# Performance work log

Measured on AMD Instinct MI355X. Metric: run time of the kernel, lower is better.

Reference implementation:

```python
import jax, jax.numpy as jnp
import numpy as np


def conv2d(x, w, b, pad=0, groups=1):
    y = jax.lax.conv_general_dilated(
        x, w, (1, 1), [(pad, pad), (pad, pad)],
        dimension_numbers=('NCHW', 'OIHW', 'NCHW'), feature_group_count=groups)
    return y + b[None, :, None, None]


def layernorm(x, w, b, eps=1e-5):
    # per-pixel LayerNorm over channel dim (matches to_3d -> nn.LayerNorm(dim) -> to_4d)
    mu = x.mean(1, keepdims=True)
    var = ((x - mu) ** 2).mean(1, keepdims=True)
    return (x - mu) * jax.lax.rsqrt(var + eps) * w[None, :, None, None] + b[None, :, None, None]


def setup_inputs():
    key = jax.random.key(0)
    ks = jax.random.split(key, 16)
    B, C, H, W = 1, 64, 64, 64
    heads, dh = 8, 8
    inner = heads * dh          # 64
    hid_lc = 32                 # max(16, inner // 2)
    hid_f = 4 * C               # 256, ffn_expansion_factor = 4
    def s(k, shape, fan):
        return (jax.random.normal(k, shape, jnp.float32) / np.float32(np.sqrt(fan)))
    return {
        'x': jax.random.normal(ks[0], (B, C, H, W), jnp.float32),
        'luma': jax.random.uniform(ks[1], (B, 1, H, W), jnp.float32),
        'ln1_w': jnp.ones((C,), jnp.float32), 'ln1_b': jnp.zeros((C,), jnp.float32),
        'qkv_w': s(ks[2], (3 * inner, C, 1, 1), C), 'qkv_b': jnp.zeros((3 * inner,), jnp.float32),
        'proj_w': s(ks[3], (C, inner, 1, 1), inner), 'proj_b': jnp.zeros((C,), jnp.float32),
        'lc1_w': s(ks[4], (hid_lc, 1, 3, 3), 9), 'lc1_b': jnp.zeros((hid_lc,), jnp.float32),
        'lc2_w': s(ks[5], (hid_lc, hid_lc, 3, 3), 9 * hid_lc), 'lc2_b': jnp.zeros((hid_lc,), jnp.float32),
        'gam_w': s(ks[6], (inner, hid_lc, 1, 1), hid_lc), 'gam_b': jnp.zeros((inner,), jnp.float32),
        'bet_w': s(ks[7], (inner, hid_lc, 1, 1), hid_lc), 'bet_b': jnp.zeros((inner,), jnp.float32),
        'alpha': jnp.float32(0.1),
        'ln2_w': jnp.ones((C,), jnp.float32), 'ln2_b': jnp.zeros((C,), jnp.float32),
        'ffn1_w': s(ks[8], (hid_f, C, 1, 1), C), 'ffn1_b': jnp.zeros((hid_f,), jnp.float32),
        'dw_w': s(ks[9], (hid_f, 1, 3, 3), 9), 'dw_b': jnp.zeros((hid_f,), jnp.float32),
        'ffn2_w': s(ks[10], (C, hid_f, 1, 1), hid_f), 'ffn2_b': jnp.zeros((C,), jnp.float32),
    }


def reference(x, luma, ln1_w, ln1_b, qkv_w, qkv_b, proj_w, proj_b,
              lc1_w, lc1_b, lc2_w, lc2_b, gam_w, gam_b, bet_w, bet_b, alpha,
              ln2_w, ln2_b, ffn1_w, ffn1_b, dw_w, dw_b, ffn2_w, ffn2_b):
    B, C, H, W = x.shape
    heads = 8
    N = H * W
    # --- attention branch ---
    xn = layernorm(x, ln1_w, ln1_b)
    qkv = conv2d(xn, qkv_w, qkv_b)             # [B, 3*inner, H, W]
    inner = qkv.shape[1] // 3
    dh = inner // heads

    def to_bhnd(t):  # b (h d) x y -> b h (x y) d
        return t.reshape(B, heads, dh, N).transpose(0, 1, 3, 2)

    q, k, v = [to_bhnd(t) for t in jnp.split(qkv, 3, axis=1)]
    # luma conditioning
    h1 = jax.nn.relu(conv2d(luma, lc1_w, lc1_b, pad=1))
    h1 = jax.nn.relu(conv2d(h1, lc2_w, lc2_b, pad=1))
    g = to_bhnd(conv2d(h1, gam_w, gam_b))
    bt = to_bhnd(conv2d(h1, bet_w, bet_b))
    q = g * q + bt
    k = g * k + bt
    v = g * v + bt
    # additive luma bias on q (avg_pool2d 3x3, count_include_pad=True -> fixed /9)
    invL = 1.0 - luma
    invL = jax.lax.reduce_window(invL, 0.0, jax.lax.add, (1, 1, 3, 3), (1, 1, 1, 1),
                                 [(0, 0), (0, 0), (1, 1), (1, 1)]) / 9.0
    invL = invL.reshape(B, N)
    invL = invL - invL.mean(-1, keepdims=True)
    q = q + alpha * invL[:, None, :, None]
    scale = dh ** -0.5
    attn = jax.nn.softmax(jnp.einsum('bhid,bhjd->bhij', q, k) * scale, axis=-1)
    out = jnp.einsum('bhij,bhjd->bhid', attn, v)
    out = out.transpose(0, 1, 3, 2).reshape(B, inner, H, W)
    x = x + conv2d(out, proj_w, proj_b)
    # --- ConvFFN branch ---
    y = layernorm(x, ln2_w, ln2_b)
    y = conv2d(y, ffn1_w, ffn1_b)
    y = conv2d(y, dw_w, dw_b, pad=1, groups=y.shape[1])
    y = jax.nn.gelu(y, approximate=False)
    y = conv2d(y, ffn2_w, ffn2_b)
    return x + y
```

## Files before the change

kernel.cpp:

```cpp
#include <hip/hip_runtime.h>
#include <math.h>

#define NPIX 4096
#define IMG 64

typedef __attribute__((ext_vector_type(8))) short bf16x8;
typedef __attribute__((ext_vector_type(4))) float floatx4;
typedef __attribute__((ext_vector_type(4))) unsigned int uintx4;

__device__ __forceinline__ unsigned int split_pack(float x) {
  unsigned int u = __float_as_uint(x);
  unsigned int hif = u & 0xffff0000u;
  float lof = x - __uint_as_float(hif);
  return (u >> 16) | (__float_as_uint(lof) & 0xffff0000u);
}

__device__ __forceinline__ unsigned int pack_hi2(float a, float b) {
  return __builtin_amdgcn_perm(__float_as_uint(b), __float_as_uint(a),
                               0x07060302u);
}

__global__ __launch_bounds__(256) void lc12_kernel(
    const float* __restrict__ luma, const float* __restrict__ w1,
    const float* __restrict__ b1, const float* __restrict__ w2,
    const float* __restrict__ b2, const float* __restrict__ x,
    float* __restrict__ h2, float* __restrict__ pooled,
    float* __restrict__ bsums, float* __restrict__ mu1,
    float* __restrict__ rs1, unsigned short* __restrict__ cbuf) {
  __shared__ float lum[400];
  __shared__ float sw1[288];
  __shared__ float tin[32][324];
  __shared__ float swt[4][32][9];
  __shared__ float red[256];
  int tile = blockIdx.x, ocg = blockIdx.y;
  int ty0 = (tile >> 2) * 16, tx0 = (tile & 3) * 16;
  int tid = threadIdx.x;
  if (tile == 0 && ocg == 0 && tid < 16) cbuf[tid] = (tid < 8) ? 0x3F80 : 0;
  for (int idx = tid; idx < 400; idx += 256) {
    int py = idx / 20, px = idx - py * 20;
    int gy = ty0 + py - 2, gx = tx0 + px - 2;
    lum[idx] = (gy >= 0 && gy < IMG && gx >= 0 && gx < IMG)
                   ? luma[gy * IMG + gx]
                   : 0.f;
  }
  for (int idx = tid; idx < 288; idx += 256) sw1[idx] = w1[idx];
  for (int idx = tid; idx < 1152; idx += 256) {
    int o = idx / 288, r = idx - o * 288;
    swt[o][r / 9][r % 9] = w2[(ocg * 4 + o) * 288 + r];
  }
  __syncthreads();
  for (int idx = tid; idx < 32 * 324; idx += 256) {
    int ic = idx / 324, pos = idx - ic * 324;
    int py = pos / 18, px = pos - py * 18;
    int gy = ty0 + py - 1, gx = tx0 + px - 1;
    float v = 0.f;
    if (gy >= 0 && gy < IMG && gx >= 0 && gx < IMG) {
      float s = b1[ic];
      const float* wp = &sw1[ic * 9];
#pragma unroll
      for (int dy = 0; dy < 3; dy++)
#pragma unroll
        for (int dx = 0; dx < 3; dx++)
          s = fmaf(wp[dy * 3 + dx], lum[(py + dy) * 20 + px + dx], s);
      v = fmaxf(s, 0.f);
    }
    tin[ic][pos] = v;
  }
  __syncthreads();
  int ly = tid >> 4, lx = tid & 15;
  int p = (ty0 + ly) * IMG + tx0 + lx;
  float acc[4];
#pragma unroll
  for (int o = 0; o < 4; o++) acc[o] = b2[ocg * 4 + o];
  for (int ic = 0; ic < 32; ic++) {
    float v[9];
#pragma unroll
    for (int dy = 0; dy < 3; dy++)
#pragma unroll
      for (int dx = 0; dx < 3; dx++)
        v[dy * 3 + dx] = tin[ic][(ly + dy) * 18 + lx + dx];
#pragma unroll
    for (int o = 0; o < 4; o++)
#pragma unroll
      for (int t = 0; t < 9; t++) acc[o] = fmaf(swt[o][ic][t], v[t], acc[o]);
  }
#pragma unroll
  for (int o = 0; o < 4; o++)
    h2[(ocg * 4 + o) * NPIX + p] = fmaxf(acc[o], 0.f);
  if (ocg == 0) {
    int gy = ty0 + ly, gx = tx0 + lx;
    float sv = 0.f;
#pragma unroll
    for (int dy = 0; dy < 3; dy++)
#pragma unroll
      for (int dx = 0; dx < 3; dx++)
        sv += lum[(ly + dy + 1) * 20 + lx + dx + 1];
    float cy = 3.f - (gy == 0 ? 1.f : 0.f) - (gy == 63 ? 1.f : 0.f);
    float cx = 3.f - (gx == 0 ? 1.f : 0.f) - (gx == 63 ? 1.f : 0.f);
    float pv = (cy * cx - sv) * (1.f / 9.f);
    pooled[p] = pv;
    red[tid] = pv;
    __syncthreads();
    for (int st = 128; st > 0; st >>= 1) {
      if (tid < st) red[tid] += red[tid + st];
      __syncthreads();
    }
    if (tid == 0) bsums[tile] = red[0];
    float s = 0.f, q = 0.f;
#pragma unroll 8
    for (int cc = 0; cc < 64; cc++) {
      float xv = x[cc * NPIX + p];
      s += xv;
      q = fmaf(xv, xv, q);
    }
    float mu = s * (1.f / 64.f);
    mu1[p] = mu;
    rs1[p] = rsqrtf(q * (1.f / 64.f) - mu * mu + 1e-5f);
  }
}

__global__ __launch_bounds__(256) void ln_qkv_kernel(
    const float* __restrict__ X, const float* __restrict__ mu1,
    const float* __restrict__ rs1, const float* __restrict__ lnw,
    const float* __restrict__ lnb, const float* __restrict__ W,
    const float* __restrict__ bias, const float* __restrict__ gamW,
    const float* __restrict__ gamB, const float* __restrict__ betW,
    const float* __restrict__ betB, const float* __restrict__ h2,
    const float* __restrict__ pooled, const float* __restrict__ bsums,
    const float* __restrict__ alpha, unsigned short* __restrict__ qhl,
    unsigned short* __restrict__ khl, unsigned short* __restrict__ vthx,
    unsigned short* __restrict__ vtlx) {
  const float QSCALE = 0.35355339059327376f * 1.4426950408889634f;
  __shared__ float xs[64][32];
  __shared__ float wsh[64][64];
  __shared__ float h2s[32][32];
  __shared__ float wgs[32][64];
  __shared__ float wbs[32][64];
  __shared__ float mu[32];
  __shared__ float rs[32];
  int n0 = blockIdx.x * 32, part = blockIdx.y, m0 = part * 64;
  int tid = threadIdx.x;
  if (tid < 32) {
    mu[tid] = mu1[n0 + tid];
    rs[tid] = rs1[n0 + tid];
  }
  {
    int e = tid * 2;
    int c = e >> 3, off = (e & 7) * 4;
    *(float4*)&xs[c][off] = *(const float4*)&X[c * NPIX + n0 + off];
    int e1 = e + 1;
    int c1 = e1 >> 3, off1 = (e1 & 7) * 4;
    *(float4*)&xs[c1][off1] = *(const float4*)&X[c1 * NPIX + n0 + off1];
  }
  {
    int m = tid >> 2, kg = (tid & 3) * 16;
    const float4* wr = (const float4*)&W[(m0 + m) * 64 + kg];
    float4 w0 = wr[0], w1 = wr[1], w2 = wr[2], w3 = wr[3];
    float wv[16] = {w0.x, w0.y, w0.z, w0.w, w1.x, w1.y, w1.z, w1.w,
                    w2.x, w2.y, w2.z, w2.w, w3.x, w3.y, w3.z, w3.w};
#pragma unroll
    for (int j = 0; j < 16; j++) wsh[kg + j][m] = wv[j];
  }
  {
    int k = tid >> 3, nf = (tid & 7) * 4;
    *(float4*)&h2s[k][nf] = *(const float4*)&h2[k * NPIX + n0 + nf];
  }
  {
    int m = tid >> 2, kg = (tid & 3) * 8;
    const float4* g0 = (const float4*)&gamW[m * 32 + kg];
    float4 a = g0[0], b4 = g0[1];
    float gv[8] = {a.x, a.y, a.z, a.w, b4.x, b4.y, b4.z, b4.w};
#pragma unroll
    for (int j = 0; j < 8; j++) wgs[kg + j][m] = gv[j];
    const float4* bb0 = (const float4*)&betW[m * 32 + kg];
    float4 c4 = bb0[0], d4 = bb0[1];
    float bv[8] = {c4.x, c4.y, c4.z, c4.w, d4.x, d4.y, d4.z, d4.w};
#pragma unroll
    for (int j = 0; j < 8; j++) wbs[kg + j][m] = bv[j];
  }
  __syncthreads();
  {
    int c = tid >> 2, pg = (tid & 3) * 8;
    float wc = lnw[c], bc = lnb[c];
#pragma unroll
    for (int j = 0; j < 8; j++) {
      int p = pg + j;
      xs[c][p] = (xs[c][p] - mu[p]) * rs[p] * wc + bc;
    }
  }
  __syncthreads();
  int tx = tid & 15, ty = tid >> 4;
  float ga[4][2] = {}, ba[4][2] = {};
#pragma unroll 8
  for (int kk = 0; kk < 32; kk++) {
    float4 wg4 = *(const float4*)&wgs[kk][ty * 4];
    float4 wb4 = *(const float4*)&wbs[kk][ty * 4];
    float2 h22 = *(const float2*)&h2s[kk][tx * 2];
    float gv[4] = {wg4.x, wg4.y, wg4.z, wg4.w};
    float bv[4] = {wb4.x, wb4.y, wb4.z, wb4.w};
    float hv[2] = {h22.x, h22.y};
#pragma unroll
    for (int im = 0; im < 4; im++)
#pragma unroll
      for (int in = 0; in < 2; in++) {
        ga[im][in] = fmaf(gv[im], hv[in], ga[im][in]);
        ba[im][in] = fmaf(bv[im], hv[in], ba[im][in]);
      }
  }
#pragma unroll
  for (int im = 0; im < 4; im++) {
    int cc = ty * 4 + im;
    float gb = gamB[cc], bb2 = betB[cc];
#pragma unroll
    for (int in = 0; in < 2; in++) {
      ga[im][in] += gb;
      ba[im][in] += bb2;
    }
  }
  float acc[4][2] = {};
#pragma unroll 8
  for (int kk = 0; kk < 64; kk++) {
    float4 a = *(const float4*)&wsh[kk][ty * 4];
    float2 b2 = *(const float2*)&xs[kk][tx * 2];
    float av[4] = {a.x, a.y, a.z, a.w};
    float bv[2] = {b2.x, b2.y};
#pragma unroll
    for (int im = 0; im < 4; im++)
#pragma unroll
      for (int in = 0; in < 2; in++)
        acc[im][in] = fmaf(av[im], bv[in], acc[im][in]);
  }
  float val[4][2];
#pragma unroll
  for (int im = 0; im < 4; im++) {
    int cc = ty * 4 + im;
    float bv = bias[m0 + cc];
#pragma unroll
    for (int in = 0; in < 2; in++)
      val[im][in] = fmaf(ga[im][in], acc[im][in] + bv, ba[im][in]);
  }
  if (part == 0) {
    float msum = 0.f;
#pragma unroll
    for (int t = 0; t < 16; t++) msum += bsums[t];
    float mean = msum * (1.f / 4096.f);
    float a0 = alpha[0];
    const float2 pv = *(const float2*)&pooled[n0 + tx * 2];
    float iv[2] = {a0 * (pv.x - mean), a0 * (pv.y - mean)};
#pragma unroll
    for (int im = 0; im < 4; im++)
#pragma unroll
      for (int in = 0; in < 2; in++)
        val[im][in] = (val[im][in] + iv[in]) * QSCALE;
  }
  if (part < 2) {
    unsigned short* dst = (part == 0) ? qhl : khl;
    int h = ty >> 1, d0 = (ty & 1) * 4;
#pragma unroll
    for (int in = 0; in < 2; in++) {
      int n = n0 + tx * 2 + in;
      unsigned int pk[4];
#pragma unroll
      for (int im = 0; im < 4; im++) pk[im] = split_pack(val[im][in]);
      short4 hi, lo;
      hi.x = (short)(pk[0] & 0xffffu); hi.y = (short)(pk[1] & 0xffffu);
      hi.z = (short)(pk[2] & 0xffffu); hi.w = (short)(pk[3] & 0xffffu);
      lo.x = (short)(pk[0] >> 16); lo.y = (short)(pk[1] >> 16);
      lo.z = (short)(pk[2] >> 16); lo.w = (short)(pk[3] >> 16);
      unsigned short* base = dst + ((size_t)(h * NPIX + n) << 4) + d0;
      *(short4*)base = hi;
      *(short4*)(base + 8) = lo;
    }
  } else {
    int nq = n0 + tx * 2;
    int off0 = (nq >> 5) * 32 + ((nq >> 4) & 1) * 4 + ((nq >> 2) & 3) * 8 +
               (nq & 3);
#pragma unroll
    for (int im = 0; im < 4; im++) {
      int cc = ty * 4 + im;
      unsigned int pk0 = split_pack(val[im][0]);
      unsigned int pk1 = split_pack(val[im][1]);
      short2 hi, lo;
      hi.x = (short)(pk0 & 0xffffu);
      hi.y = (short)(pk1 & 0xffffu);
      lo.x = (short)(pk0 >> 16);
      lo.y = (short)(pk1 >> 16);
      *(short2*)(vthx + (size_t)cc * NPIX + off0) = hi;
      *(short2*)(vtlx + (size_t)cc * NPIX + off0) = lo;
    }
  }
}

__global__ __launch_bounds__(256, 4) void attn_kernel(
    const unsigned short* __restrict__ qhl,
    const unsigned short* __restrict__ khl,
    const unsigned short* __restrict__ vthx,
    const unsigned short* __restrict__ vtlx,
    const unsigned short* __restrict__ cbuf, float* __restrict__ pacc,
    float* __restrict__ pl) {
  int tid = threadIdx.x;
  int wave = tid >> 6, lane = tid & 63;
  int g = lane >> 4, c = lane & 15;
  int h = blockIdx.y, jp = blockIdx.z;
  int i0 = blockIdx.x * 256 + wave * 64;
  int jbase = jp * 512;
  bf16x8 qB[4];
#pragma unroll
  for (int t = 0; t < 4; t++)
    qB[t] = *(const bf16x8*)(qhl + ((size_t)(h * NPIX + i0 + t * 16 + c) << 4) +
                             ((g & 1) << 3));
  const unsigned short* kp =
      khl + ((size_t)(h * NPIX + jbase + c) << 4) + ((g >> 1) << 3);
  const unsigned short* vhp;
  const unsigned short* vlp;
  int vstep;
  if (c < 8) {
    vhp = vthx + (size_t)(h * 8 + c) * NPIX + jbase + (g << 3);
    vlp = vtlx + (size_t)(h * 8 + c) * NPIX + jbase + (g << 3);
    vstep = 32;
  } else {
    vhp = (c == 8) ? cbuf : (cbuf + 8);
    vlp = cbuf + 8;
    vstep = 0;
  }
  floatx4 zero4 = {0.f, 0.f, 0.f, 0.f};
  floatx4 aH[4], aM[4];
#pragma unroll
  for (int t = 0; t < 4; t++) {
    aH[t] = zero4;
    aM[t] = zero4;
  }
#pragma unroll 4
  for (int jt = 0; jt < 16; ++jt) {
    bf16x8 ka0 = *(const bf16x8*)kp;
    bf16x8 ka1 = *(const bf16x8*)(kp + 256);
    bf16x8 avh = *(const bf16x8*)vhp;
    bf16x8 avl = *(const bf16x8*)vlp;
    kp += 512;
    vhp += vstep;
    vlp += vstep;
#pragma unroll
    for (int t = 0; t < 4; t++) {
      floatx4 s0 =
          __builtin_amdgcn_mfma_f32_16x16x32_bf16(ka0, qB[t], zero4, 0, 0, 0);
      floatx4 s1 =
          __builtin_amdgcn_mfma_f32_16x16x32_bf16(ka1, qB[t], zero4, 0, 0, 0);
      float p0 = __builtin_amdgcn_exp2f(fminf(s0[0], 80.f));
      float p1 = __builtin_amdgcn_exp2f(fminf(s0[1], 80.f));
      float p2 = __builtin_amdgcn_exp2f(fminf(s0[2], 80.f));
      float p3 = __builtin_amdgcn_exp2f(fminf(s0[3], 80.f));
      float p4 = __builtin_amdgcn_exp2f(fminf(s1[0], 80.f));
      float p5 = __builtin_amdgcn_exp2f(fminf(s1[1], 80.f));
      float p6 = __builtin_amdgcn_exp2f(fminf(s1[2], 80.f));
      float p7 = __builtin_amdgcn_exp2f(fminf(s1[3], 80.f));
      uintx4 bh;
      bh.x = pack_hi2(p0, p1);
      bh.y = pack_hi2(p2, p3);
      bh.z = pack_hi2(p4, p5);
      bh.w = pack_hi2(p6, p7);
      bf16x8 pbh = __builtin_bit_cast(bf16x8, bh);
      aH[t] = __builtin_amdgcn_mfma_f32_16x16x32_bf16(avh, pbh, aH[t], 0, 0, 0);
      aM[t] = __builtin_amdgcn_mfma_f32_16x16x32_bf16(avl, pbh, aM[t], 0, 0, 0);
    }
  }
#pragma unroll
  for (int t = 0; t < 4; t++) {
    floatx4 o = aH[t] + aM[t];
    if (g < 2) {
      size_t b0 = (size_t)((jp * 8 + h) * NPIX + i0 + t * 16 + c);
      *(float4*)&pacc[b0 * 8 + g * 4] = make_float4(o[0], o[1], o[2], o[3]);
    } else if (g == 2) {
      pl[(size_t)((jp * 8 + h) * NPIX + i0 + t * 16 + c)] = o[0];
    }
  }
}

__global__ __launch_bounds__(256) void proj_ffn1_kernel(
    const float* __restrict__ pacc, const float* __restrict__ pl,
    const float* __restrict__ Wp, const float* __restrict__ bp,
    const float* __restrict__ x, const float* __restrict__ ln2w,
    const float* __restrict__ ln2b, const float* __restrict__ W1,
    const float* __restrict__ b1f, float* __restrict__ x1,
    float* __restrict__ f1) {
  __shared__ float at[64][34];
  __shared__ float wsh[64][68];
  __shared__ float w1s[64][68];
  __shared__ float xsl[64][34];
  __shared__ float ps[16][34];
  __shared__ float pq[16][34];
  __shared__ float mus[32];
  __shared__ float rss[32];
  int n0 = blockIdx.x * 32;
  int ch = blockIdx.y;
  int tid = threadIdx.x;
  {
    int mm = tid >> 2, kg = (tid & 3) * 16;
    const float4* wr = (const float4*)&Wp[mm * 64 + kg];
    float4 w0 = wr[0], w1 = wr[1], w2 = wr[2], w3 = wr[3];
    float wv[16] = {w0.x, w0.y, w0.z, w0.w, w1.x, w1.y, w1.z, w1.w,
                    w2.x, w2.y, w2.z, w2.w, w3.x, w3.y, w3.z, w3.w};
#pragma unroll
    for (int j = 0; j < 16; j++) wsh[kg + j][mm] = wv[j];
    const float4* w1r = (const float4*)&W1[(ch * 64 + mm) * 64 + kg];
    float4 u0 = w1r[0], u1 = w1r[1], u2 = w1r[2], u3 = w1r[3];
    float uv[16] = {u0.x, u0.y, u0.z, u0.w, u1.x, u1.y, u1.z, u1.w,
                    u2.x, u2.y, u2.z, u2.w, u3.x, u3.y, u3.z, u3.w};
#pragma unroll
    for (int j = 0; j < 16; j++) w1s[kg + j][mm] = uv[j];
  }
  {
    int hh = tid >> 5, nn = tid & 31;
    int i = n0 + nn;
    float L = 0.f, o[8] = {};
#pragma unroll
    for (int p = 0; p < 8; p++) {
      size_t base = (size_t)((p * 8 + hh) * NPIX + i);
      L += pl[base];
      const float4 a0 = *(const float4*)&pacc[base * 8];
      const float4 a1 = *(const float4*)&pacc[base * 8 + 4];
      o[0] += a0.x; o[1] += a0.y; o[2] += a0.z; o[3] += a0.w;
      o[4] += a1.x; o[5] += a1.y; o[6] += a1.z; o[7] += a1.w;
    }
    float inv = 1.f / L;
#pragma unroll
    for (int d = 0; d < 8; d++) at[hh * 8 + d][nn] = o[d] * inv;
  }
  __syncthreads();
  int mq = tid >> 4, pp = (tid & 15) * 2;
  float acc[4][2] = {};
#pragma unroll 8
  for (int k = 0; k < 64; k++) {
    float4 w4 = *(const float4*)&wsh[k][mq * 4];
    float2 b2 = *(const float2*)&at[k][pp];
    acc[0][0] = fmaf(w4.x, b2.x, acc[0][0]);
    acc[0][1] = fmaf(w4.x, b2.y, acc[0][1]);
    acc[1][0] = fmaf(w4.y, b2.x, acc[1][0]);
    acc[1][1] = fmaf(w4.y, b2.y, acc[1][1]);
    acc[2][0] = fmaf(w4.z, b2.x, acc[2][0]);
    acc[2][1] = fmaf(w4.z, b2.y, acc[2][1]);
    acc[3][0] = fmaf(w4.w, b2.x, acc[3][0]);
    acc[3][1] = fmaf(w4.w, b2.y, acc[3][1]);
  }
  float v[4][2], sn0 = 0.f, sn1 = 0.f, qn0 = 0.f, qn1 = 0.f;
#pragma unroll
  for (int im = 0; im < 4; im++) {
    int row = mq * 4 + im;
    float bpv = bp[row];
    const float2 xr = *(const float2*)&x[row * NPIX + n0 + pp];
    float v0 = acc[im][0] + bpv + xr.x;
    float v1 = acc[im][1] + bpv + xr.y;
    v[im][0] = v0;
    v[im][1] = v1;
    sn0 += v0;
    qn0 = fmaf(v0, v0, qn0);
    sn1 += v1;
    qn1 = fmaf(v1, v1, qn1);
  }
  if (ch == 0) {
#pragma unroll
    for (int im = 0; im < 4; im++)
      *(float2*)&x1[(mq * 4 + im) * NPIX + n0 + pp] =
          make_float2(v[im][0], v[im][1]);
  }
  ps[mq][pp] = sn0;
  ps[mq][pp + 1] = sn1;
  pq[mq][pp] = qn0;
  pq[mq][pp + 1] = qn1;
  __syncthreads();
  if (tid < 32) {
    float s = 0.f, q = 0.f;
#pragma unroll
    for (int t = 0; t < 16; t++) {
      s += ps[t][tid];
      q += pq[t][tid];
    }
    float mu = s * (1.f / 64.f);
    mus[tid] = mu;
    rss[tid] = rsqrtf(q * (1.f / 64.f) - mu * mu + 1e-5f);
  }
  __syncthreads();
  {
    float mu0 = mus[pp], mu1v = mus[pp + 1];
    float rs0 = rss[pp], rs1v = rss[pp + 1];
#pragma unroll
    for (int im = 0; im < 4; im++) {
      int row = mq * 4 + im;
      float w2v = ln2w[row], b2v = ln2b[row];
      *(float2*)&xsl[row][pp] =
          make_float2((v[im][0] - mu0) * rs0 * w2v + b2v,
                      (v[im][1] - mu1v) * rs1v * w2v + b2v);
    }
  }
  __syncthreads();
  float a2[4][2] = {};
#pragma unroll 8
  for (int k = 0; k < 64; k++) {
    float4 w4 = *(const float4*)&w1s[k][mq * 4];
    float2 b2 = *(const float2*)&xsl[k][pp];
    a2[0][0] = fmaf(w4.x, b2.x, a2[0][0]);
    a2[0][1] = fmaf(w4.x, b2.y, a2[0][1]);
    a2[1][0] = fmaf(w4.y, b2.x, a2[1][0]);
    a2[1][1] = fmaf(w4.y, b2.y, a2[1][1]);
    a2[2][0] = fmaf(w4.z, b2.x, a2[2][0]);
    a2[2][1] = fmaf(w4.z, b2.y, a2[2][1]);
    a2[3][0] = fmaf(w4.w, b2.x, a2[3][0]);
    a2[3][1] = fmaf(w4.w, b2.y, a2[3][1]);
  }
#pragma unroll
  for (int im = 0; im < 4; im++) {
    int row = ch * 64 + mq * 4 + im;
    float bb = b1f[row];
    *(float2*)&f1[row * NPIX + n0 + pp] =
        make_float2(a2[im][0] + bb, a2[im][1] + bb);
  }
}

__global__ __launch_bounds__(256) void ffn2_dw_kernel(
    const float* __restrict__ f1, const float* __restrict__ dww,
    const float* __restrict__ dwb, const float* __restrict__ W,
    const float* __restrict__ bias, const float* __restrict__ resid,
    float* __restrict__ C) {
  __shared__ float xs2[16][260];
  __shared__ float wshT[32][260];
  int n0 = blockIdx.x * 16, m0 = blockIdx.y * 32;
  int tid = threadIdx.x;
  int y = n0 >> 6, x0 = n0 & 63;
  {
    int mm = tid >> 3, kg = (tid & 7) * 32;
    const float4* src = (const float4*)&W[(m0 + mm) * 256 + kg];
    float4* dst = (float4*)&wshT[mm][kg];
#pragma unroll
    for (int i = 0; i < 8; i++) dst[i] = src[i];
  }
  {
    int px4 = (tid & 3) * 4;
    int xabs = x0 + px4;
#pragma unroll
    for (int k = 0; k < 4; k++) {
      int c = (tid >> 2) + 64 * k;
      const float* base = f1 + c * NPIX;
      float wv[9];
#pragma unroll
      for (int i = 0; i < 9; i++) wv[i] = dww[c * 9 + i];
      float bc = dwb[c];
      float a[4] = {bc, bc, bc, bc};
#pragma unroll
      for (int dy = 0; dy < 3; dy++) {
        int yy = y + dy - 1;
        if (yy < 0 || yy > 63) continue;
        const float* row = base + yy * IMG + xabs;
        float4 mid = *(const float4*)row;
        float left = (xabs > 0) ? row[-1] : 0.f;
        float right = (xabs + 4 < IMG) ? row[4] : 0.f;
        float win[6] = {left, mid.x, mid.y, mid.z, mid.w, right};
#pragma unroll
        for (int o = 0; o < 4; o++)
#pragma unroll
          for (int dx = 0; dx < 3; dx++)
            a[o] = fmaf(wv[dy * 3 + dx], win[o + dx], a[o]);
      }
#pragma unroll
      for (int o = 0; o < 4; o++)
        xs2[px4 + o][c] =
            0.5f * a[o] * (1.f + erff(a[o] * 0.70710678118654752f));
    }
  }
  __syncthreads();
  int m = tid >> 3, np = (tid & 7) * 2;
  float a0 = 0.f, a1 = 0.f;
#pragma unroll 4
  for (int k4 = 0; k4 < 64; k4++) {
    float4 w4 = *(const float4*)&wshT[m][k4 * 4];
    float4 xa = *(const float4*)&xs2[np][k4 * 4];
    float4 xb = *(const float4*)&xs2[np + 1][k4 * 4];
    a0 = fmaf(w4.x, xa.x, a0);
    a1 = fmaf(w4.x, xb.x, a1);
    a0 = fmaf(w4.y, xa.y, a0);
    a1 = fmaf(w4.y, xb.y, a1);
    a0 = fmaf(w4.z, xa.z, a0);
    a1 = fmaf(w4.z, xb.z, a1);
    a0 = fmaf(w4.w, xa.w, a0);
    a1 = fmaf(w4.w, xb.w, a1);
  }
  int row = m0 + m;
  float bv = bias[row];
  const float2 rr = *(const float2*)&resid[row * NPIX + n0 + np];
  *(float2*)&C[row * NPIX + n0 + np] =
      make_float2(a0 + bv + rr.x, a1 + bv + rr.y);
}

extern "C" void kernel_launch(void* const* d_in, const int* in_sizes, int n_in,
                              void* d_out, int out_size, void* d_ws,
                              size_t ws_size, hipStream_t stream) {
  const float* x      = (const float*)d_in[0];
  const float* luma   = (const float*)d_in[1];
  const float* ln1_w  = (const float*)d_in[2];
  const float* ln1_b  = (const float*)d_in[3];
  const float* qkv_w  = (const float*)d_in[4];
  const float* qkv_b  = (const float*)d_in[5];
  const float* proj_w = (const float*)d_in[6];
  const float* proj_b = (const float*)d_in[7];
  const float* lc1_w  = (const float*)d_in[8];
  const float* lc1_b  = (const float*)d_in[9];
  const float* lc2_w  = (const float*)d_in[10];
  const float* lc2_b  = (const float*)d_in[11];
  const float* gam_w  = (const float*)d_in[12];
  const float* gam_b  = (const float*)d_in[13];
  const float* bet_w  = (const float*)d_in[14];
  const float* bet_b  = (const float*)d_in[15];
  const float* alpha  = (const float*)d_in[16];
  const float* ln2_w  = (const float*)d_in[17];
  const float* ln2_b  = (const float*)d_in[18];
  const float* ffn1_w = (const float*)d_in[19];
  const float* ffn1_b = (const float*)d_in[20];
  const float* dw_w   = (const float*)d_in[21];
  const float* dw_b   = (const float*)d_in[22];
  const float* ffn2_w = (const float*)d_in[23];
  const float* ffn2_b = (const float*)d_in[24];
  float* out = (float*)d_out;

  float* w = (float*)d_ws;
  float* pooled = w + 0;
  float* bsums  = w + 4096;
  unsigned short* cbuf = (unsigned short*)(w + 4160);
  float* mu1 = w + 4224;
  float* rs1 = w + 8320;
  unsigned short* qhl  = (unsigned short*)(w + 12416);
  unsigned short* khl  = (unsigned short*)(w + 274560);
  unsigned short* vthx = (unsigned short*)(w + 536704);
  unsigned short* vtlx = (unsigned short*)(w + 667776);
  float* pacc = w + 798848;
  float* pl   = w + 2896000;
  float* x1   = w + 3158144;
  float* f1   = w + 3420288;
  float* h2   = w + 4468864;

  lc12_kernel<<<dim3(16, 8), 256, 0, stream>>>(luma, lc1_w, lc1_b, lc2_w,
                                               lc2_b, x, h2, pooled, bsums,
                                               mu1, rs1, cbuf);
  ln_qkv_kernel<<<dim3(128, 3), 256, 0, stream>>>(
      x, mu1, rs1, ln1_w, ln1_b, qkv_w, qkv_b, gam_w, gam_b, bet_w, bet_b, h2,
      pooled, bsums, alpha, qhl, khl, vthx, vtlx);
  attn_kernel<<<dim3(16, 8, 8), 256, 0, stream>>>(qhl, khl, vthx, vtlx, cbuf,
                                                  pacc, pl);
  proj_ffn1_kernel<<<dim3(128, 4), 256, 0, stream>>>(
      pacc, pl, proj_w, proj_b, x, ln2_w, ln2_b, ffn1_w, ffn1_b, x1, f1);
  ffn2_dw_kernel<<<dim3(256, 2), 256, 0, stream>>>(f1, dw_w, dw_b, ffn2_w,
                                                   ffn2_b, x1, out);
}
```

Baseline: 190.7 us.

## Fuse all stages into one persistent kernel with global atomic barriers

Replaces the five separate kernel launches with a single persistent 512-block kernel. Each stage is selected by block index, and a software grid barrier built on an atomic counter separates the stages. Shared memory is unioned across stages, and a tiny init kernel resets the counters and cbuf. This aims to remove launch overhead and inter-kernel gaps. In exchange it relies on all 512 blocks being co-resident to avoid deadlock, and the spin-wait barriers plus fixed per-stage grids may leave some blocks idle.

```diff
diff --git a/kernel.cpp b/kernel.cpp
--- a/kernel.cpp
+++ b/kernel.cpp
@@ -3,6 +3,7 @@
 
 #define NPIX 4096
 #define IMG 64
+#define NBLK 512
 
 typedef __attribute__((ext_vector_type(8))) short bf16x8;
 typedef __attribute__((ext_vector_type(4))) float floatx4;
@@ -20,573 +21,629 @@
                                0x07060302u);
 }
 
-__global__ __launch_bounds__(256) void lc12_kernel(
-    const float* __restrict__ luma, const float* __restrict__ w1,
-    const float* __restrict__ b1, const float* __restrict__ w2,
-    const float* __restrict__ b2, const float* __restrict__ x,
-    float* __restrict__ h2, float* __restrict__ pooled,
-    float* __restrict__ bsums, float* __restrict__ mu1,
-    float* __restrict__ rs1, unsigned short* __restrict__ cbuf) {
-  __shared__ float lum[400];
-  __shared__ float sw1[288];
-  __shared__ float tin[32][324];
-  __shared__ float swt[4][32][9];
-  __shared__ float red[256];
-  int tile = blockIdx.x, ocg = blockIdx.y;
-  int ty0 = (tile >> 2) * 16, tx0 = (tile & 3) * 16;
-  int tid = threadIdx.x;
-  if (tile == 0 && ocg == 0 && tid < 16) cbuf[tid] = (tid < 8) ? 0x3F80 : 0;
-  for (int idx = tid; idx < 400; idx += 256) {
-    int py = idx / 20, px = idx - py * 20;
-    int gy = ty0 + py - 2, gx = tx0 + px - 2;
-    lum[idx] = (gy >= 0 && gy < IMG && gx >= 0 && gx < IMG)
-                   ? luma[gy * IMG + gx]
-                   : 0.f;
-  }
-  for (int idx = tid; idx < 288; idx += 256) sw1[idx] = w1[idx];
-  for (int idx = tid; idx < 1152; idx += 256) {
-    int o = idx / 288, r = idx - o * 288;
-    swt[o][r / 9][r % 9] = w2[(ocg * 4 + o) * 288 + r];
+__device__ __forceinline__ void gbar(unsigned int* ctr) {
+  __syncthreads();
+  __threadfence();
+  if (threadIdx.x == 0) {
+    atomicAdd(ctr, 1u);
+    while (__hip_atomic_load(ctr, __ATOMIC_RELAXED,
+                             __HIP_MEMORY_SCOPE_AGENT) < (unsigned)NBLK)
+      __builtin_amdgcn_s_sleep(2);
   }
   __syncthreads();
-  for (int idx = tid; idx < 32 * 324; idx += 256) {
-    int ic = idx / 324, pos = idx - ic * 324;
-    int py = pos / 18, px = pos - py * 18;
-    int gy = ty0 + py - 1, gx = tx0 + px - 1;
-    float v = 0.f;
-    if (gy >= 0 && gy < IMG && gx >= 0 && gx < IMG) {
-      float s = b1[ic];
-      const float* wp = &sw1[ic * 9];
+  __threadfence();
+}
+
+struct S1 {
+  float lum[400];
+  float sw1[288];
+  float tin[32][324];
+  float swt[4][32][9];
+  float red[256];
+};
+struct S2 {
+  float xs[64][32];
+  float wsh[64][64];
+  float h2s[32][32];
+  float wgs[32][64];
+  float wbs[32][64];
+  float mu[32];
+  float rs[32];
+};
+struct S4 {
+  float at[64][34];
+  float wsh[64][64];
+  float xsl[64][34];
+  float ps[16][32];
+  float pq[16][32];
+  float mus[32];
+  float rss[32];
+};
+struct S5 {
+  float xs2[16][260];
+  float wshT[32][260];
+};
+union SU {
+  S1 s1;
+  S2 s2;
+  S4 s4;
+  S5 s5;
+};
+
+__global__ void init_kernel(unsigned int* __restrict__ ctr,
+                            unsigned short* __restrict__ cbuf) {
+  int t = threadIdx.x;
+  if (t < 8) ctr[t] = 0u;
+  if (t >= 32 && t < 48) cbuf[t - 32] = (t - 32 < 8) ? 0x3F80 : 0;
+}
+
+__global__ __launch_bounds__(256, 3) void fused_kernel(
+    const float* __restrict__ x, const float* __restrict__ luma,
+    const float* __restrict__ lc1w, const float* __restrict__ lc1b,
+    const float* __restrict__ lc2w, const float* __restrict__ lc2b,
+    const float* __restrict__ ln1w, const float* __restrict__ ln1b,
+    const float* __restrict__ qkvW, const float* __restrict__ qkvB,
+    const float* __restrict__ gamW, const float* __restrict__ gamB,
+    const float* __restrict__ betW, const float* __restrict__ betB,
+    const float* __restrict__ alpha, const float* __restrict__ projW,
+    const float* __restrict__ projB, const float* __restrict__ ln2w,
+    const float* __restrict__ ln2b, const float* __restrict__ ffn1W,
+    const float* __restrict__ ffn1B, const float* __restrict__ dww,
+    const float* __restrict__ dwb, const float* __restrict__ ffn2W,
+    const float* __restrict__ ffn2B, float* __restrict__ out,
+    float* __restrict__ pooled, float* __restrict__ bsums,
+    unsigned short* __restrict__ cbuf, float* __restrict__ mu1,
+    float* __restrict__ rs1, unsigned short* __restrict__ qhl,
+    unsigned short* __restrict__ khl, unsigned short* __restrict__ vthx,
+    unsigned short* __restrict__ vtlx, float* __restrict__ pacc,
+    float* __restrict__ pl, float* __restrict__ x1, float* __restrict__ f1,
+    float* __restrict__ h2, unsigned int* __restrict__ ctr) {
+  __shared__ SU u;
+  int bid = blockIdx.x;
+  int tid = threadIdx.x;
+
+  if (bid < 128) {
+    int tile = bid >> 3, ocg = bid & 7;
+    int ty0 = (tile >> 2) * 16, tx0 = (tile & 3) * 16;
+    float(&lum)[400] = u.s1.lum;
+    float(&sw1)[288] = u.s1.sw1;
+    float(&tin)[32][324] = u.s1.tin;
+    float(&swt)[4][32][9] = u.s1.swt;
+    float(&red)[256] = u.s1.red;
+    for (int idx = tid; idx < 400; idx += 256) {
+      int py = idx / 20, px = idx - py * 20;
+      int gy = ty0 + py - 2, gx = tx0 + px - 2;
+      lum[idx] = (gy >= 0 && gy < IMG && gx >= 0 && gx < IMG)
+                     ? luma[gy * IMG + gx]
+                     : 0.f;
+    }
+    for (int idx = tid; idx < 288; idx += 256) sw1[idx] = lc1w[idx];
+    for (int idx = tid; idx < 1152; idx += 256) {
+      int o = idx / 288, r = idx - o * 288;
+      swt[o][r / 9][r % 9] = lc2w[(ocg * 4 + o) * 288 + r];
+    }
+    __syncthreads();
+    for (int idx = tid; idx < 32 * 324; idx += 256) {
+      int ic = idx / 324, pos = idx - ic * 324;
+      int py = pos / 18, px = pos - py * 18;
+      int gy = ty0 + py - 1, gx = tx0 + px - 1;
+      float v = 0.f;
+      if (gy >= 0 && gy < IMG && gx >= 0 && gx < IMG) {
+        float s = lc1b[ic];
+        const float* wp = &sw1[ic * 9];
+#pragma unroll
+        for (int dy = 0; dy < 3; dy++)
+#pragma unroll
+          for (int dx = 0; dx < 3; dx++)
+            s = fmaf(wp[dy * 3 + dx], lum[(py + dy) * 20 + px + dx], s);
+        v = fmaxf(s, 0.f);
+      }
+      tin[ic][pos] = v;
+    }
+    __syncthreads();
+    int ly = tid >> 4, lx = tid & 15;
+    int p = (ty0 + ly) * IMG + tx0 + lx;
+    float acc[4];
+#pragma unroll
+    for (int o = 0; o < 4; o++) acc[o] = lc2b[ocg * 4 + o];
+    for (int ic = 0; ic < 32; ic++) {
+      float v[9];
 #pragma unroll
       for (int dy = 0; dy < 3; dy++)
 #pragma unroll
         for (int dx = 0; dx < 3; dx++)
-          s = fmaf(wp[dy * 3 + dx], lum[(py + dy) * 20 + px + dx], s);
-      v = fmaxf(s, 0.f);
-    }
-    tin[ic][pos] = v;
+          v[dy * 3 + dx] = tin[ic][(ly + dy) * 18 + lx + dx];
+#pragma unroll
+      for (int o = 0; o < 4; o++)
+#pragma unroll
+        for (int t = 0; t < 9; t++) acc[o] = fmaf(swt[o][ic][t], v[t], acc[o]);
+    }
+#pragma unroll
+    for (int o = 0; o < 4; o++)
+      h2[(ocg * 4 + o) * NPIX + p] = fmaxf(acc[o], 0.f);
+    if (ocg == 0) {
+      int gy = ty0 + ly, gx = tx0 + lx;
+      float sv = 0.f;
+#pragma unroll
+      for (int dy = 0; dy < 3; dy++)
+#pragma unroll
+        for (int dx = 0; dx < 3; dx++)
+          sv += lum[(ly + dy + 1) * 20 + lx + dx + 1];
+      float cy = 3.f - (gy == 0 ? 1.f : 0.f) - (gy == 63 ? 1.f : 0.f);
+      float cx = 3.f - (gx == 0 ? 1.f : 0.f) - (gx == 63 ? 1.f : 0.f);
+      float pv = (cy * cx - sv) * (1.f / 9.f);
+      pooled[p] = pv;
+      red[tid] = pv;
+      __syncthreads();
+      for (int st = 128; st > 0; st >>= 1) {
+        if (tid < st) red[tid] += red[tid + st];
+        __syncthreads();
+      }
+      if (tid == 0) bsums[tile] = red[0];
+      float s = 0.f, q = 0.f;
+#pragma unroll 8
+      for (int cc = 0; cc < 64; cc++) {
+        float xv = x[cc * NPIX + p];
+        s += xv;
+        q = fmaf(xv, xv, q);
+      }
+      float mu = s * (1.f / 64.f);
+      mu1[p] = mu;
+      rs1[p] = rsqrtf(q * (1.f / 64.f) - mu * mu + 1e-5f);
+    }
   }
-  __syncthreads();
-  int ly = tid >> 4, lx = tid & 15;
-  int p = (ty0 + ly) * IMG + tx0 + lx;
-  float acc[4];
-#pragma unroll
-  for (int o = 0; o < 4; o++) acc[o] = b2[ocg * 4 + o];
-  for (int ic = 0; ic < 32; ic++) {
-    float v[9];
-#pragma unroll
-    for (int dy = 0; dy < 3; dy++)
-#pragma unroll
-      for (int dx = 0; dx < 3; dx++)
-        v[dy * 3 + dx] = tin[ic][(ly + dy) * 18 + lx + dx];
-#pragma unroll
-    for (int o = 0; o < 4; o++)
-#pragma unroll
-      for (int t = 0; t < 9; t++) acc[o] = fmaf(swt[o][ic][t], v[t], acc[o]);
-  }
-#pragma unroll
-  for (int o = 0; o < 4; o++)
-    h2[(ocg * 4 + o) * NPIX + p] = fmaxf(acc[o], 0.f);
-  if (ocg == 0) {
-    int gy = ty0 + ly, gx = tx0 + lx;
-    float sv = 0.f;
-#pragma unroll
-    for (int dy = 0; dy < 3; dy++)
-#pragma unroll
-      for (int dx = 0; dx < 3; dx++)
-        sv += lum[(ly + dy + 1) * 20 + lx + dx + 1];
-    float cy = 3.f - (gy == 0 ? 1.f : 0.f) - (gy == 63 ? 1.f : 0.f);
-    float cx = 3.f - (gx == 0 ? 1.f : 0.f) - (gx == 63 ? 1.f : 0.f);
-    float pv = (cy * cx - sv) * (1.f / 9.f);
-    pooled[p] = pv;
-    red[tid] = pv;
-    __syncthreads();
-    for (int st = 128; st > 0; st >>= 1) {
-      if (tid < st) red[tid] += red[tid + st];
-      __syncthreads();
-    }
-    if (tid == 0) bsums[tile] = red[0];
-    float s = 0.f, q = 0.f;
+  gbar(&ctr[0]);
+
+  if (bid < 384) {
+    const float QSCALE = 0.35355339059327376f * 1.4426950408889634f;
+    float(&xs)[64][32] = u.s2.xs;
+    float(&wsh)[64][64] = u.s2.wsh;
+    float(&h2s)[32][32] = u.s2.h2s;
+    float(&wgs)[32][64] = u.s2.wgs;
+    float(&wbs)[32][64] = u.s2.wbs;
+    float(&mu)[32] = u.s2.mu;
+    float(&rs)[32] = u.s2.rs;
+    int n0 = (bid & 127) * 32, part = bid >> 7, m0 = part * 64;
+    if (tid < 32) {
+      mu[tid] = mu1[n0 + tid];
+      rs[tid] = rs1[n0 + tid];
+    }
+    {
+      int e = tid * 2;
+      int c = e >> 3, off = (e & 7) * 4;
+      *(float4*)&xs[c][off] = *(const float4*)&x[c * NPIX + n0 + off];
+      int e1 = e + 1;
+      int c1 = e1 >> 3, off1 = (e1 & 7) * 4;
+      *(float4*)&xs[c1][off1] = *(const float4*)&x[c1 * NPIX + n0 + off1];
+    }
+    {
+      int m = tid >> 2, kg = (tid & 3) * 16;
+      const float4* wr = (const float4*)&qkvW[(m0 + m) * 64 + kg];
+      float4 w0 = wr[0], w1 = wr[1], w2 = wr[2], w3 = wr[3];
+      float wv[16] = {w0.x, w0.y, w0.z, w0.w, w1.x, w1.y, w1.z, w1.w,
+                      w2.x, w2.y, w2.z, w2.w, w3.x, w3.y, w3.z, w3.w};
+#pragma unroll
+      for (int j = 0; j < 16; j++) wsh[kg + j][m] = wv[j];
+    }
+    {
+      int k = tid >> 3, nf = (tid & 7) * 4;
+      *(float4*)&h2s[k][nf] = *(const float4*)&h2[k * NPIX + n0 + nf];
+    }
+    {
+      int m = tid >> 2, kg = (tid & 3) * 8;
+      const float4* g0 = (const float4*)&gamW[m * 32 + kg];
+      float4 a = g0[0], b4 = g0[1];
+      float gv[8] = {a.x, a.y, a.z, a.w, b4.x, b4.y, b4.z, b4.w};
+#pragma unroll
+      for (int j = 0; j < 8; j++) wgs[kg + j][m] = gv[j];
+      const float4* bb0 = (const float4*)&betW[m * 32 + kg];
+      float4 c4 = bb0[0], d4 = bb0[1];
+      float bv[8] = {c4.x, c4.y, c4.z, c4.w, d4.x, d4.y, d4.z, d4.w};
+#pragma unroll
+      for (int j = 0; j < 8; j++) wbs[kg + j][m] = bv[j];
+    }
+    __syncthreads();
+    {
+      int c = tid >> 2, pg = (tid & 3) * 8;
+      float wc = ln1w[c], bc = ln1b[c];
+#pragma unroll
+      for (int j = 0; j < 8; j++) {
+        int p = pg + j;
+        xs[c][p] = (xs[c][p] - mu[p]) * rs[p] * wc + bc;
+      }
+    }
+    __syncthreads();
+    int tx = tid & 15, ty = tid >> 4;
+    float ga[4][2] = {}, ba[4][2] = {};
 #pragma unroll 8
-    for (int cc = 0; cc < 64; cc++) {
-      float xv = x[cc * NPIX + p];
-      s += xv;
-      q = fmaf(xv, xv, q);
-    }
-    float mu = s * (1.f / 64.f);
-    mu1[p] = mu;
-    rs1[p] = rsqrtf(q * (1.f / 64.f) - mu * mu + 1e-5f);
-  }
-}
-
-__global__ __launch_bounds__(256) void ln_qkv_kernel(
-    const float* __restrict__ X, const float* __restrict__ mu1,
-    const float* __restrict__ rs1, const float* __restrict__ lnw,
-    const float* __restrict__ lnb, const float* __restrict__ W,
-    const float* __restrict__ bias, const float* __restrict__ gamW,
-    const float* __restrict__ gamB, const float* __restrict__ betW,
-    const float* __restrict__ betB, const float* __restrict__ h2,
-    const float* __restrict__ pooled, const float* __restrict__ bsums,
-    const float* __restrict__ alpha, unsigned short* __restrict__ qhl,
-    unsigned short* __restrict__ khl, unsigned short* __restrict__ vthx,
-    unsigned short* __restrict__ vtlx) {
-  const float QSCALE = 0.35355339059327376f * 1.4426950408889634f;
-  __shared__ float xs[64][32];
-  __shared__ float wsh[64][64];
-  __shared__ float h2s[32][32];
-  __shared__ float wgs[32][64];
-  __shared__ float wbs[32][64];
-  __shared__ float mu[32];
-  __shared__ float rs[32];
-  int n0 = blockIdx.x * 32, part = blockIdx.y, m0 = part * 64;
-  int tid = threadIdx.x;
-  if (tid < 32) {
-    mu[tid] = mu1[n0 + tid];
-    rs[tid] = rs1[n0 + tid];
-  }
-  {
-    int e = tid * 2;
-    int c = e >> 3, off = (e & 7) * 4;
-    *(float4*)&xs[c][off] = *(const float4*)&X[c * NPIX + n0 + off];
-    int e1 = e + 1;
-    int c1 = e1 >> 3, off1 = (e1 & 7) * 4;
-    *(float4*)&xs[c1][off1] = *(const float4*)&X[c1 * NPIX + n0 + off1];
-  }
-  {
-    int m = tid >> 2, kg = (tid & 3) * 16;
-    const float4* wr = (const float4*)&W[(m0 + m) * 64 + kg];
-    float4 w0 = wr[0], w1 = wr[1], w2 = wr[2], w3 = wr[3];
-    float wv[16] = {w0.x, w0.y, w0.z, w0.w, w1.x, w1.y, w1.z, w1.w,
-                    w2.x, w2.y, w2.z, w2.w, w3.x, w3.y, w3.z, w3.w};
-#pragma unroll
-    for (int j = 0; j < 16; j++) wsh[kg + j][m] = wv[j];
-  }
-  {
-    int k = tid >> 3, nf = (tid & 7) * 4;
-    *(float4*)&h2s[k][nf] = *(const float4*)&h2[k * NPIX + n0 + nf];
-  }
-  {
-    int m = tid >> 2, kg = (tid & 3) * 8;
-    const float4* g0 = (const float4*)&gamW[m * 32 + kg];
-    float4 a = g0[0], b4 = g0[1];
-    float gv[8] = {a.x, a.y, a.z, a.w, b4.x, b4.y, b4.z, b4.w};
-#pragma unroll
-    for (int j = 0; j < 8; j++) wgs[kg + j][m] = gv[j];
-    const float4* bb0 = (const float4*)&betW[m * 32 + kg];
-    float4 c4 = bb0[0], d4 = bb0[1];
-    float bv[8] = {c4.x, c4.y, c4.z, c4.w, d4.x, d4.y, d4.z, d4.w};
-#pragma unroll
-    for (int j = 0; j < 8; j++) wbs[kg + j][m] = bv[j];
-  }
-  __syncthreads();
-  {
-    int c = tid >> 2, pg = (tid & 3) * 8;
-    float wc = lnw[c], bc = lnb[c];
-#pragma unroll
-    for (int j = 0; j < 8; j++) {
-      int p = pg + j;
-      xs[c][p] = (xs[c][p] - mu[p]) * rs[p] * wc + bc;
-    }
-  }
-  __syncthreads();
-  int tx = tid & 15, ty = tid >> 4;
-  float ga[4][2] = {}, ba[4][2] = {};
-#pragma unroll 8
-  for (int kk = 0; kk < 32; kk++) {
-    float4 wg4 = *(const float4*)&wgs[kk][ty * 4];
-    float4 wb4 = *(const float4*)&wbs[kk][ty * 4];
-    float2 h22 = *(const float2*)&h2s[kk][tx * 2];
-    float gv[4] = {wg4.x, wg4.y, wg4.z, wg4.w};
-    float bv[4] = {wb4.x, wb4.y, wb4.z, wb4.w};
-    float hv[2] = {h22.x, h22.y};
-#pragma unroll
-    for (int im = 0; im < 4; im++)
-#pragma unroll
-      for (int in = 0; in < 2; in++) {
-        ga[im][in] = fmaf(gv[im], hv[in], ga[im][in]);
-        ba[im][in] = fmaf(bv[im], hv[in], ba[im][in]);
-      }
-  }
-#pragma unroll
-  for (int im = 0; im < 4; im++) {
-    int cc = ty * 4 + im;
-    float gb = gamB[cc], bb2 = betB[cc];
-#pragma unroll
-    for (int in = 0; in < 2; in++) {
-      ga[im][in] += gb;
-      ba[im][in] += bb2;
-    }
-  }
-  float acc[4][2] = {};
-#pragma unroll 8
-  for (int kk = 0; kk < 64; kk++) {
-    float4 a = *(const float4*)&wsh[kk][ty * 4];
-    float2 b2 = *(const float2*)&xs[kk][tx * 2];
-    float av[4] = {a.x, a.y, a.z, a.w};
-    float bv[2] = {b2.x, b2.y};
-#pragma unroll
-    for (int im = 0; im < 4; im++)
-#pragma unroll
-      for (int in = 0; in < 2; in++)
-        acc[im][in] = fmaf(av[im], bv[in], acc[im][in]);
-  }
-  float val[4][2];
-#pragma unroll
-  for (int im = 0; im < 4; im++) {
-    int cc = ty * 4 + im;
-    float bv = bias[m0 + cc];
-#pragma unroll
-    for (int in = 0; in < 2; in++)
-      val[im][in] = fmaf(ga[im][in], acc[im][in] + bv, ba[im][in]);
-  }
-  if (part == 0) {
-    float msum = 0.f;
-#pragma unroll
-    for (int t = 0; t < 16; t++) msum += bsums[t];
-    float mean = msum * (1.f / 4096.f);
-    float a0 = alpha[0];
-    const float2 pv = *(const float2*)&pooled[n0 + tx * 2];
-    float iv[2] = {a0 * (pv.x - mean), a0 * (pv.y - mean)};
-#pragma unroll
-    for (int im = 0; im < 4; im++)
-#pragma unroll
-      for (int in = 0; in < 2; in++)
-        val[im][in] = (val[im][in] + iv[in]) * QSCALE;
-  }
-  if (part < 2) {
-    unsigned short* dst = (part == 0) ? qhl : khl;
-    int h = ty >> 1, d0 = (ty & 1) * 4;
-#pragma unroll
-    for (int in = 0; in < 2; in++) {
-      int n = n0 + tx * 2 + in;
-      unsigned int pk[4];
-#pragma unroll
-      for (int im = 0; im < 4; im++) pk[im] = split_pack(val[im][in]);
-      short4 hi, lo;
-      hi.x = (short)(pk[0] & 0xffffu); hi.y = (short)(pk[1] & 0xffffu);
-      hi.z = (short)(pk[2] & 0xffffu); hi.w = (short)(pk[3] & 0xffffu);
-      lo.x = (short)(pk[0] >> 16); lo.y = (short)(pk[1] >> 16);
-      lo.z = (short)(pk[2] >> 16); lo.w = (short)(pk[3] >> 16);
-      unsigned short* base = dst + ((size_t)(h * NPIX + n) << 4) + d0;
-      *(short4*)base = hi;
-      *(short4*)(base + 8) = lo;
-    }
-  } else {
-    int nq = n0 + tx * 2;
-    int off0 = (nq >> 5) * 32 + ((nq >> 4) & 1) * 4 + ((nq >> 2) & 3) * 8 +
-               (nq & 3);
+    for (int kk = 0; kk < 32; kk++) {
+      float4 wg4 = *(const float4*)&wgs[kk][ty * 4];
+      float4 wb4 = *(const float4*)&wbs[kk][ty * 4];
+      float2 h22 = *(const float2*)&h2s[kk][tx * 2];
+      float gv[4] = {wg4.x, wg4.y, wg4.z, wg4.w};
+      float bv[4] = {wb4.x, wb4.y, wb4.z, wb4.w};
+      float hv[2] = {h22.x, h22.y};
+#pragma unroll
+      for (int im = 0; im < 4; im++)
+#pragma unroll
+        for (int in = 0; in < 2; in++) {
+          ga[im][in] = fmaf(gv[im], hv[in], ga[im][in]);
+          ba[im][in] = fmaf(bv[im], hv[in], ba[im][in]);
+        }
+    }
 #pragma unroll
     for (int im = 0; im < 4; im++) {
       int cc = ty * 4 + im;
-      unsigned int pk0 = split_pack(val[im][0]);
-      unsigned int pk1 = split_pack(val[im][1]);
-      short2 hi, lo;
-      hi.x = (short)(pk0 & 0xffffu);
-      hi.y = (short)(pk1 & 0xffffu);
-      lo.x = (short)(pk0 >> 16);
-      lo.y = (short)(pk1 >> 16);
-      *(short2*)(vthx + (size_t)cc * NPIX + off0) = hi;
-      *(short2*)(vtlx + (size_t)cc * NPIX + off0) = lo;
+      float gb = gamB[cc], bb2 = betB[cc];
+#pragma unroll
+      for (int in = 0; in < 2; in++) {
+        ga[im][in] += gb;
+        ba[im][in] += bb2;
+      }
+    }
+    float acc[4][2] = {};
+#pragma unroll 8
+    for (int kk = 0; kk < 64; kk++) {
+      float4 a = *(const float4*)&wsh[kk][ty * 4];
+      float2 b2 = *(const float2*)&xs[kk][tx * 2];
+      float av[4] = {a.x, a.y, a.z, a.w};
+      float bv[2] = {b2.x, b2.y};
+#pragma unroll
+      for (int im = 0; im < 4; im++)
+#pragma unroll
+        for (int in = 0; in < 2; in++)
+          acc[im][in] = fmaf(av[im], bv[in], acc[im][in]);
+    }
+    float val[4][2];
+#pragma unroll
+    for (int im = 0; im < 4; im++) {
+      int cc = ty * 4 + im;
+      float bv = qkvB[m0 + cc];
+#pragma unroll
+      for (int in = 0; in < 2; in++)
+        val[im][in] = fmaf(ga[im][in], acc[im][in] + bv, ba[im][in]);
+    }
+    if (part == 0) {
+      float msum = 0.f;
+#pragma unroll
+      for (int t = 0; t < 16; t++) msum += bsums[t];
+      float mean = msum * (1.f / 4096.f);
+      float a0 = alpha[0];
+      const float2 pv = *(const float2*)&pooled[n0 + tx * 2];
+      float iv[2] = {a0 * (pv.x - mean), a0 * (pv.y - mean)};
+#pragma unroll
+      for (int im = 0; im < 4; im++)
+#pragma unroll
+        for (int in = 0; in < 2; in++)
+          val[im][in] = (val[im][in] + iv[in]) * QSCALE;
+    }
+    if (part < 2) {
+      unsigned short* dst = (part == 0) ? qhl : khl;
+      int hh = ty >> 1, d0 = (ty & 1) * 4;
+#pragma unroll
+      for (int in = 0; in < 2; in++) {
+        int n = n0 + tx * 2 + in;
+        unsigned int pk[4];
+#pragma unroll
+        for (int im = 0; im < 4; im++) pk[im] = split_pack(val[im][in]);
+        short4 hi, lo;
+        hi.x = (short)(pk[0] & 0xffffu); hi.y = (short)(pk[1] & 0xffffu);
+        hi.z = (short)(pk[2] & 0xffffu); hi.w = (short)(pk[3] & 0xffffu);
+        lo.x = (short)(pk[0] >> 16); lo.y = (short)(pk[1] >> 16);
+        lo.z = (short)(pk[2] >> 16); lo.w = (short)(pk[3] >> 16);
+        unsigned short* base = dst + ((size_t)(hh * NPIX + n) << 4) + d0;
+        *(short4*)base = hi;
+        *(short4*)(base + 8) = lo;
+      }
+    } else {
+      int nq = n0 + tx * 2;
+      int off0 = (nq >> 5) * 32 + ((nq >> 4) & 1) * 4 + ((nq >> 2) & 3) * 8 +
+                 (nq & 3);
+#pragma unroll
+      for (int im = 0; im < 4; im++) {
+        int cc = ty * 4 + im;
+        unsigned int pk0 = split_pack(val[im][0]);
+        unsigned int pk1 = split_pack(val[im][1]);
+        short2 hi, lo;
+        hi.x = (short)(pk0 & 0xffffu);
+        hi.y = (short)(pk1 & 0xffffu);
+        lo.x = (short)(pk0 >> 16);
+        lo.y = (short)(pk1 >> 16);
+        *(short2*)(vthx + (size_t)cc * NPIX + off0) = hi;
+        *(short2*)(vtlx + (size_t)cc * NPIX + off0) = lo;
+      }
     }
   }
-}
-
-__global__ __launch_bounds__(256, 4) void attn_kernel(
-    const unsigned short* __restrict__ qhl,
-    const unsigned short* __restrict__ khl,
-    const unsigned short* __restrict__ vthx,
-    const unsigned short* __restrict__ vtlx,
-    const unsigned short* __restrict__ cbuf, float* __restrict__ pacc,
-    float* __restrict__ pl) {
-  int tid = threadIdx.x;
-  int wave = tid >> 6, lane = tid & 63;
-  int g = lane >> 4, c = lane & 15;
-  int h = blockIdx.y, jp = blockIdx.z;
-  int i0 = blockIdx.x * 256 + wave * 64;
-  int jbase = jp * 512;
-  bf16x8 qB[4];
-#pragma unroll
-  for (int t = 0; t < 4; t++)
-    qB[t] = *(const bf16x8*)(qhl + ((size_t)(h * NPIX + i0 + t * 16 + c) << 4) +
-                             ((g & 1) << 3));
-  const unsigned short* kp =
-      khl + ((size_t)(h * NPIX + jbase + c) << 4) + ((g >> 1) << 3);
-  const unsigned short* vhp;
-  const unsigned short* vlp;
-  int vstep;
-  if (c < 8) {
-    vhp = vthx + (size_t)(h * 8 + c) * NPIX + jbase + (g << 3);
-    vlp = vtlx + (size_t)(h * 8 + c) * NPIX + jbase + (g << 3);
-    vstep = 32;
-  } else {
-    vhp = (c == 8) ? cbuf : (cbuf + 8);
-    vlp = cbuf + 8;
-    vstep = 0;
+  gbar(&ctr[1]);
+
+  {
+    int wave = tid >> 6, lane = tid & 63;
+    int g = lane >> 4, c = lane & 15;
+#pragma unroll 1
+    for (int rep = 0; rep < 2; rep++) {
+      int unit = bid * 2 + rep;
+      int h = (unit >> 4) & 7, jp = unit >> 7;
+      int i0 = (unit & 15) * 256 + wave * 64;
+      int jbase = jp * 512;
+      bf16x8 qB[4];
+#pragma unroll
+      for (int t = 0; t < 4; t++)
+        qB[t] = *(const bf16x8*)(qhl +
+                                 ((size_t)(h * NPIX + i0 + t * 16 + c) << 4) +
+                                 ((g & 1) << 3));
+      const unsigned short* kp =
+          khl + ((size_t)(h * NPIX + jbase + c) << 4) + ((g >> 1) << 3);
+      const unsigned short* vhp;
+      const unsigned short* vlp;
+      int vstep;
+      if (c < 8) {
+        vhp = vthx + (size_t)(h * 8 + c) * NPIX + jbase + (g << 3);
+        vlp = vtlx + (size_t)(h * 8 + c) * NPIX + jbase + (g << 3);
+        vstep = 32;
+      } else {
+        vhp = (c == 8) ? cbuf : (cbuf + 8);
+        vlp = cbuf + 8;
+        vstep = 0;
+      }
+      floatx4 zero4 = {0.f, 0.f, 0.f, 0.f};
+      floatx4 aH[4], aM[4];
+#pragma unroll
+      for (int t = 0; t < 4; t++) {
+        aH[t] = zero4;
+        aM[t] = zero4;
+      }
+#pragma unroll 4
+      for (int jt = 0; jt < 16; ++jt) {
+        bf16x8 ka0 = *(const bf16x8*)kp;
+        bf16x8 ka1 = *(const bf16x8*)(kp + 256);
+        bf16x8 avh = *(const bf16x8*)vhp;
+        bf16x8 avl = *(const bf16x8*)vlp;
+        kp += 512;
+        vhp += vstep;
+        vlp += vstep;
+#pragma unroll
+        for (int t = 0; t < 4; t++) {
+          floatx4 s0 = __builtin_amdgcn_mfma_f32_16x16x32_bf16(ka0, qB[t],
+                                                               zero4, 0, 0, 0);
+          floatx4 s1 = __builtin_amdgcn_mfma_f32_16x16x32_bf16(ka1, qB[t],
+                                                               zero4, 0, 0, 0);
+          float p0 = __builtin_amdgcn_exp2f(fminf(s0[0], 80.f));
+          float p1 = __builtin_amdgcn_exp2f(fminf(s0[1], 80.f));
+          float p2 = __builtin_amdgcn_exp2f(fminf(s0[2], 80.f));
+          float p3 = __builtin_amdgcn_exp2f(fminf(s0[3], 80.f));
+          float p4 = __builtin_amdgcn_exp2f(fminf(s1[0], 80.f));
+          float p5 = __builtin_amdgcn_exp2f(fminf(s1[1], 80.f));
+          float p6 = __builtin_amdgcn_exp2f(fminf(s1[2], 80.f));
+          float p7 = __builtin_amdgcn_exp2f(fminf(s1[3], 80.f));
+          uintx4 bh;
+          bh.x = pack_hi2(p0, p1);
+          bh.y = pack_hi2(p2, p3);
+          bh.z = pack_hi2(p4, p5);
+          bh.w = pack_hi2(p6, p7);
+          bf16x8 pbh = __builtin_bit_cast(bf16x8, bh);
+          aH[t] =
+              __builtin_amdgcn_mfma_f32_16x16x32_bf16(avh, pbh, aH[t], 0, 0, 0);
+          aM[t] =
+              __builtin_amdgcn_mfma_f32_16x16x32_bf16(avl, pbh, aM[t], 0, 0, 0);
+        }
+      }
+#pragma unroll
+      for (int t = 0; t < 4; t++) {
+        floatx4 o = aH[t] + aM[t];
+        if (g < 2) {
+          size_t b0 = (size_t)((jp * 8 + h) * NPIX + i0 + t * 16 + c);
+          *(float4*)&pacc[b0 * 8 + g * 4] = make_float4(o[0], o[1], o[2], o[3]);
+        } else if (g == 2) {
+          pl[(size_t)((jp * 8 + h) * NPIX + i0 + t * 16 + c)] = o[0];
+        }
+      }
+    }
   }
-  floatx4 zero4 = {0.f, 0.f, 0.f, 0.f};
-  floatx4 aH[4], aM[4];
-#pragma unroll
-  for (int t = 0; t < 4; t++) {
-    aH[t] = zero4;
-    aM[t] = zero4;
-  }
-#pragma unroll 4
-  for (int jt = 0; jt < 16; ++jt) {
-    bf16x8 ka0 = *(const bf16x8*)kp;
-    bf16x8 ka1 = *(const bf16x8*)(kp + 256);
-    bf16x8 avh = *(const bf16x8*)vhp;
-    bf16x8 avl = *(const bf16x8*)vlp;
-    kp += 512;
-    vhp += vstep;
-    vlp += vstep;
-#pragma unroll
-    for (int t = 0; t < 4; t++) {
-      floatx4 s0 =
-          __builtin_amdgcn_mfma_f32_16x16x32_bf16(ka0, qB[t], zero4, 0, 0, 0);
-      floatx4 s1 =
-          __builtin_amdgcn_mfma_f32_16x16x32_bf16(ka1, qB[t], zero4, 0, 0, 0);
-      float p0 = __builtin_amdgcn_exp2f(fminf(s0[0], 80.f));
-      float p1 = __builtin_amdgcn_exp2f(fminf(s0[1], 80.f));
-      float p2 = __builtin_amdgcn_exp2f(fminf(s0[2], 80.f));
-      float p3 = __builtin_amdgcn_exp2f(fminf(s0[3], 80.f));
-      float p4 = __builtin_amdgcn_exp2f(fminf(s1[0], 80.f));
-      float p5 = __builtin_amdgcn_exp2f(fminf(s1[1], 80.f));
-      float p6 = __builtin_amdgcn_exp2f(fminf(s1[2], 80.f));
-      float p7 = __builtin_amdgcn_exp2f(fminf(s1[3], 80.f));
-      uintx4 bh;
-      bh.x = pack_hi2(p0, p1);
-      bh.y = pack_hi2(p2, p3);
-      bh.z = pack_hi2(p4, p5);
-      bh.w = pack_hi2(p6, p7);
-      bf16x8 pbh = __builtin_bit_cast(bf16x8, bh);
-      aH[t] = __builtin_amdgcn_mfma_f32_16x16x32_bf16(avh, pbh, aH[t], 0, 0, 0);
-      aM[t] = __builtin_amdgcn_mfma_f32_16x16x32_bf16(avl, pbh, aM[t], 0, 0, 0);
-    }
-  }
-#pragma unroll
-  for (int t = 0; t < 4; t++) {
-    floatx4 o = aH[t] + aM[t];
-    if (g < 2) {
-      size_t b0 = (size_t)((jp * 8 + h) * NPIX + i0 + t * 16 + c);
-      *(float4*)&pacc[b0 * 8 + g * 4] = make_float4(o[0], o[1], o[2], o[3]);
-    } else if (g == 2) {
-      pl[(size_t)((jp * 8 + h) * NPIX + i0 + t * 16 + c)] = o[0];
-    }
-  }
-}
-
-__global__ __launch_bounds__(256) void proj_ffn1_kernel(
-    const float* __restrict__ pacc, const float* __restrict__ pl,
-    const float* __restrict__ Wp, const float* __restrict__ bp,
-    const float* __restrict__ x, const float* __restrict__ ln2w,
-    const float* __restrict__ ln2b, const float* __restrict__ W1,
-    const float* __restrict__ b1f, float* __restrict__ x1,
-    float* __restrict__ f1) {
-  __shared__ float at[64][34];
-  __shared__ float wsh[64][68];
-  __shared__ float w1s[64][68];
-  __shared__ float xsl[64][34];
-  __shared__ float ps[16][34];
-  __shared__ float pq[16][34];
-  __shared__ float mus[32];
-  __shared__ float rss[32];
-  int n0 = blockIdx.x * 32;
-  int ch = blockIdx.y;
-  int tid = threadIdx.x;
+  gbar(&ctr[2]);
+
   {
+    float(&at)[64][34] = u.s4.at;
+    float(&wsh)[64][64] = u.s4.wsh;
+    float(&xsl)[64][34] = u.s4.xsl;
+    float(&ps)[16][32] = u.s4.ps;
+    float(&pq)[16][32] = u.s4.pq;
+    float(&mus)[32] = u.s4.mus;
+    float(&rss)[32] = u.s4.rss;
+    int n0 = (bid & 127) * 32;
+    int ch = bid >> 7;
     int mm = tid >> 2, kg = (tid & 3) * 16;
-    const float4* wr = (const float4*)&Wp[mm * 64 + kg];
-    float4 w0 = wr[0], w1 = wr[1], w2 = wr[2], w3 = wr[3];
-    float wv[16] = {w0.x, w0.y, w0.z, w0.w, w1.x, w1.y, w1.z, w1.w,
-                    w2.x, w2.y, w2.z, w2.w, w3.x, w3.y, w3.z, w3.w};
-#pragma unroll
-    for (int j = 0; j < 16; j++) wsh[kg + j][mm] = wv[j];
-    const float4* w1r = (const float4*)&W1[(ch * 64 + mm) * 64 + kg];
-    float4 u0 = w1r[0], u1 = w1r[1], u2 = w1r[2], u3 = w1r[3];
-    float uv[16] = {u0.x, u0.y, u0.z, u0.w, u1.x, u1.y, u1.z, u1.w,
-                    u2.x, u2.y, u2.z, u2.w, u3.x, u3.y, u3.z, u3.w};
-#pragma unroll
-    for (int j = 0; j < 16; j++) w1s[kg + j][mm] = uv[j];
-  }
-  {
-    int hh = tid >> 5, nn = tid & 31;
-    int i = n0 + nn;
-    float L = 0.f, o[8] = {};
-#pragma unroll
-    for (int p = 0; p < 8; p++) {
-      size_t base = (size_t)((p * 8 + hh) * NPIX + i);
-      L += pl[base];
-      const float4 a0 = *(const float4*)&pacc[base * 8];
-      const float4 a1 = *(const float4*)&pacc[base * 8 + 4];
-      o[0] += a0.x; o[1] += a0.y; o[2] += a0.z; o[3] += a0.w;
-      o[4] += a1.x; o[5] += a1.y; o[6] += a1.z; o[7] += a1.w;
-    }
-    float inv = 1.f / L;
-#pragma unroll
-    for (int d = 0; d < 8; d++) at[hh * 8 + d][nn] = o[d] * inv;
-  }
-  __syncthreads();
-  int mq = tid >> 4, pp = (tid & 15) * 2;
-  float acc[4][2] = {};
+    {
+      const float4* wr = (const float4*)&projW[mm * 64 + kg];
+      float4 w0 = wr[0], w1 = wr[1], w2 = wr[2], w3 = wr[3];
+      float wv[16] = {w0.x, w0.y, w0.z, w0.w, w1.x, w1.y, w1.z, w1.w,
+                      w2.x, w2.y, w2.z, w2.w, w3.x, w3.y, w3.z, w3.w};
+#pragma unroll
+      for (int j = 0; j < 16; j++) wsh[kg + j][mm] = wv[j];
+    }
+    {
+      int hh = tid >> 5, nn = tid & 31;
+      int i = n0 + nn;
+      float L = 0.f, o[8] = {};
+#pragma unroll
+      for (int p = 0; p < 8; p++) {
+        size_t base = (size_t)((p * 8 + hh) * NPIX + i);
+        L += pl[base];
+        const float4 a0 = *(const float4*)&pacc[base * 8];
+        const float4 a1 = *(const float4*)&pacc[base * 8 + 4];
+        o[0] += a0.x; o[1] += a0.y; o[2] += a0.z; o[3] += a0.w;
+        o[4] += a1.x; o[5] += a1.y; o[6] += a1.z; o[7] += a1.w;
+      }
+      float inv = 1.f / L;
+#pragma unroll
+      for (int d = 0; d < 8; d++) at[hh * 8 + d][nn] = o[d] * inv;
+    }
+    __syncthreads();
+    int mq = tid >> 4, pp = (tid & 15) * 2;
+    float acc[4][2] = {};
 #pragma unroll 8
-  for (int k = 0; k < 64; k++) {
-    float4 w4 = *(const float4*)&wsh[k][mq * 4];
-    float2 b2 = *(const float2*)&at[k][pp];
-    acc[0][0] = fmaf(w4.x, b2.x, acc[0][0]);
-    acc[0][1] = fmaf(w4.x, b2.y, acc[0][1]);
-    acc[1][0] = fmaf(w4.y, b2.x, acc[1][0]);
-    acc[1][1] = fmaf(w4.y, b2.y, acc[1][1]);
-    acc[2][0] = fmaf(w4.z, b2.x, acc[2][0]);
-    acc[2][1] = fmaf(w4.z, b2.y, acc[2][1]);
-    acc[3][0] = fmaf(w4.w, b2.x, acc[3][0]);
-    acc[3][1] = fmaf(w4.w, b2.y, acc[3][1]);
-  }
-  float v[4][2], sn0 = 0.f, sn1 = 0.f, qn0 = 0.f, qn1 = 0.f;
-#pragma unroll
-  for (int im = 0; im < 4; im++) {
-    int row = mq * 4 + im;
-    float bpv = bp[row];
-    const float2 xr = *(const float2*)&x[row * NPIX + n0 + pp];
-    float v0 = acc[im][0] + bpv + xr.x;
-    float v1 = acc[im][1] + bpv + xr.y;
-    v[im][0] = v0;
-    v[im][1] = v1;
-    sn0 += v0;
-    qn0 = fmaf(v0, v0, qn0);
-    sn1 += v1;
-    qn1 = fmaf(v1, v1, qn1);
-  }
-  if (ch == 0) {
-#pragma unroll
-    for (int im = 0; im < 4; im++)
-      *(float2*)&x1[(mq * 4 + im) * NPIX + n0 + pp] =
-          make_float2(v[im][0], v[im][1]);
-  }
-  ps[mq][pp] = sn0;
-  ps[mq][pp + 1] = sn1;
-  pq[mq][pp] = qn0;
-  pq[mq][pp + 1] = qn1;
-  __syncthreads();
-  if (tid < 32) {
-    float s = 0.f, q = 0.f;
-#pragma unroll
-    for (int t = 0; t < 16; t++) {
-      s += ps[t][tid];
-      q += pq[t][tid];
-    }
-    float mu = s * (1.f / 64.f);
-    mus[tid] = mu;
-    rss[tid] = rsqrtf(q * (1.f / 64.f) - mu * mu + 1e-5f);
-  }
-  __syncthreads();
-  {
-    float mu0 = mus[pp], mu1v = mus[pp + 1];
-    float rs0 = rss[pp], rs1v = rss[pp + 1];
+    for (int k = 0; k < 64; k++) {
+      float4 w4 = *(const float4*)&wsh[k][mq * 4];
+      float2 b2 = *(const float2*)&at[k][pp];
+      acc[0][0] = fmaf(w4.x, b2.x, acc[0][0]);
+      acc[0][1] = fmaf(w4.x, b2.y, acc[0][1]);
+      acc[1][0] = fmaf(w4.y, b2.x, acc[1][0]);
+      acc[1][1] = fmaf(w4.y, b2.y, acc[1][1]);
+      acc[2][0] = fmaf(w4.z, b2.x, acc[2][0]);
+      acc[2][1] = fmaf(w4.z, b2.y, acc[2][1]);
+      acc[3][0] = fmaf(w4.w, b2.x, acc[3][0]);
+      acc[3][1] = fmaf(w4.w, b2.y, acc[3][1]);
+    }
+    float v[4][2], sn0 = 0.f, sn1 = 0.f, qn0 = 0.f, qn1 = 0.f;
 #pragma unroll
     for (int im = 0; im < 4; im++) {
       int row = mq * 4 + im;
-      float w2v = ln2w[row], b2v = ln2b[row];
-      *(float2*)&xsl[row][pp] =
-          make_float2((v[im][0] - mu0) * rs0 * w2v + b2v,
-                      (v[im][1] - mu1v) * rs1v * w2v + b2v);
+      float bpv = projB[row];
+      const float2 xr = *(const float2*)&x[row * NPIX + n0 + pp];
+      float v0 = acc[im][0] + bpv + xr.x;
+      float v1 = acc[im][1] + bpv + xr.y;
+      v[im][0] = v0;
+      v[im][1] = v1;
+      sn0 += v0;
+      qn0 = fmaf(v0, v0, qn0);
+      sn1 += v1;
+      qn1 = fmaf(v1, v1, qn1);
+    }
+    if (ch == 0) {
+#pragma unroll
+      for (int im = 0; im < 4; im++)
+        *(float2*)&x1[(mq * 4 + im) * NPIX + n0 + pp] =
+            make_float2(v[im][0], v[im][1]);
+    }
+    ps[mq][pp] = sn0;
+    ps[mq][pp + 1] = sn1;
+    pq[mq][pp] = qn0;
+    pq[mq][pp + 1] = qn1;
+    __syncthreads();
+    {
+      const float4* w1r = (const float4*)&ffn1W[(ch * 64 + mm) * 64 + kg];
+      float4 u0 = w1r[0], u1 = w1r[1], u2 = w1r[2], u3 = w1r[3];
+      float uv[16] = {u0.x, u0.y, u0.z, u0.w, u1.x, u1.y, u1.z, u1.w,
+                      u2.x, u2.y, u2.z, u2.w, u3.x, u3.y, u3.z, u3.w};
+#pragma unroll
+      for (int j = 0; j < 16; j++) wsh[kg + j][mm] = uv[j];
+    }
+    if (tid < 32) {
+      float s = 0.f, q = 0.f;
+#pragma unroll
+      for (int t = 0; t < 16; t++) {
+        s += ps[t][tid];
+        q += pq[t][tid];
+      }
+      float mu = s * (1.f / 64.f);
+      mus[tid] = mu;
+      rss[tid] = rsqrtf(q * (1.f / 64.f) - mu * mu + 1e-5f);
+    }
+    __syncthreads();
+    {
+      float mu0 = mus[pp], mu1v = mus[pp + 1];
+      float rs0 = rss[pp], rs1v = rss[pp + 1];
+#pragma unroll
+      for (int im = 0; im < 4; im++) {
+        int row = mq * 4 + im;
+        float w2v = ln2w[row], b2v = ln2b[row];
+        *(float2*)&xsl[row][pp] =
+            make_float2((v[im][0] - mu0) * rs0 * w2v + b2v,
+                        (v[im][1] - mu1v) * rs1v * w2v + b2v);
+      }
+    }
+    __syncthreads();
+    float a2[4][2] = {};
+#pragma unroll 8
+    for (int k = 0; k < 64; k++) {
+      float4 w4 = *(const float4*)&wsh[k][mq * 4];
+      float2 b2 = *(const float2*)&xsl[k][pp];
+      a2[0][0] = fmaf(w4.x, b2.x, a2[0][0]);
+      a2[0][1] = fmaf(w4.x, b2.y, a2[0][1]);
+      a2[1][0] = fmaf(w4.y, b2.x, a2[1][0]);
+      a2[1][1] = fmaf(w4.y, b2.y, a2[1][1]);
+      a2[2][0] = fmaf(w4.z, b2.x, a2[2][0]);
+      a2[2][1] = fmaf(w4.z, b2.y, a2[2][1]);
+      a2[3][0] = fmaf(w4.w, b2.x, a2[3][0]);
+      a2[3][1] = fmaf(w4.w, b2.y, a2[3][1]);
+    }
+#pragma unroll
+    for (int im = 0; im < 4; im++) {
+      int row = ch * 64 + mq * 4 + im;
+      float bb = ffn1B[row];
+      *(float2*)&f1[row * NPIX + n0 + pp] =
+          make_float2(a2[im][0] + bb, a2[im][1] + bb);
     }
   }
-  __syncthreads();
-  float a2[4][2] = {};
-#pragma unroll 8
-  for (int k = 0; k < 64; k++) {
-    float4 w4 = *(const float4*)&w1s[k][mq * 4];
-    float2 b2 = *(const float2*)&xsl[k][pp];
-    a2[0][0] = fmaf(w4.x, b2.x, a2[0][0]);
-    a2[0][1] = fmaf(w4.x, b2.y, a2[0][1]);
-    a2[1][0] = fmaf(w4.y, b2.x, a2[1][0]);
-    a2[1][1] = fmaf(w4.y, b2.y, a2[1][1]);
-    a2[2][0] = fmaf(w4.z, b2.x, a2[2][0]);
-    a2[2][1] = fmaf(w4.z, b2.y, a2[2][1]);
-    a2[3][0] = fmaf(w4.w, b2.x, a2[3][0]);
-    a2[3][1] = fmaf(w4.w, b2.y, a2[3][1]);
+  gbar(&ctr[3]);
+
+  {
+    float(&xs2)[16][260] = u.s5.xs2;
+    float(&wshT)[32][260] = u.s5.wshT;
+    int n0 = (bid & 255) * 16, m0 = (bid >> 8) * 32;
+    int y = n0 >> 6, x0 = n0 & 63;
+    {
+      int mm = tid >> 3, kg = (tid & 7) * 32;
+      const float4* src = (const float4*)&ffn2W[(m0 + mm) * 256 + kg];
+      float4* dst = (float4*)&wshT[mm][kg];
+#pragma unroll
+      for (int i = 0; i < 8; i++) dst[i] = src[i];
+    }
+    {
+      int px4 = (tid & 3) * 4;
+      int xabs = x0 + px4;
+#pragma unroll
+      for (int k = 0; k < 4; k++) {
+        int c = (tid >> 2) + 64 * k;
+        const float* base = f1 + c * NPIX;
+        float wv[9];
+#pragma unroll
+        for (int i = 0; i < 9; i++) wv[i] = dww[c * 9 + i];
+        float bc = dwb[c];
+        float a[4] = {bc, bc, bc, bc};
+#pragma unroll
+        for (int dy = 0; dy < 3; dy++) {
+          int yy = y + dy - 1;
+          if (yy < 0 || yy > 63) continue;
+          const float* row = base + yy * IMG + xabs;
+          float4 mid = *(const float4*)row;
+          float left = (xabs > 0) ? row[-1] : 0.f;
+          float right = (xabs + 4 < IMG) ? row[4] : 0.f;
+          float win[6] = {left, mid.x, mid.y, mid.z, mid.w, right};
+#pragma unroll
+          for (int o = 0; o < 4; o++)
+#pragma unroll
+            for (int dx = 0; dx < 3; dx++)
+              a[o] = fmaf(wv[dy * 3 + dx], win[o + dx], a[o]);
+        }
+#pragma unroll
+        for (int o = 0; o < 4; o++)
+          xs2[px4 + o][c] =
+              0.5f * a[o] * (1.f + erff(a[o] * 0.70710678118654752f));
+      }
+    }
+    __syncthreads();
+    int m = tid >> 3, np = (tid & 7) * 2;
+    float a0 = 0.f, a1 = 0.f;
+#pragma unroll 4
+    for (int k4 = 0; k4 < 64; k4++) {
+      float4 w4 = *(const float4*)&wshT[m][k4 * 4];
+      float4 xa = *(const float4*)&xs2[np][k4 * 4];
+      float4 xb = *(const float4*)&xs2[np + 1][k4 * 4];
+      a0 = fmaf(w4.x, xa.x, a0);
+      a1 = fmaf(w4.x, xb.x, a1);
+      a0 = fmaf(w4.y, xa.y, a0);
+      a1 = fmaf(w4.y, xb.y, a1);
+      a0 = fmaf(w4.z, xa.z, a0);
+      a1 = fmaf(w4.z, xb.z, a1);
+      a0 = fmaf(w4.w, xa.w, a0);
+      a1 = fmaf(w4.w, xb.w, a1);
+    }
+    int row = m0 + m;
+    float bv = ffn2B[row];
+    const float2 rr = *(const float2*)&x1[row * NPIX + n0 + np];
+    *(float2*)&out[row * NPIX + n0 + np] =
+        make_float2(a0 + bv + rr.x, a1 + bv + rr.y);
   }
-#pragma unroll
-  for (int im = 0; im < 4; im++) {
-    int row = ch * 64 + mq * 4 + im;
-    float bb = b1f[row];
-    *(float2*)&f1[row * NPIX + n0 + pp] =
-        make_float2(a2[im][0] + bb, a2[im][1] + bb);
-  }
-}
-
-__global__ __launch_bounds__(256) void ffn2_dw_kernel(
-    const float* __restrict__ f1, const float* __restrict__ dww,
-    const float* __restrict__ dwb, const float* __restrict__ W,
-    const float* __restrict__ bias, const float* __restrict__ resid,
-    float* __restrict__ C) {
-  __shared__ float xs2[16][260];
-  __shared__ float wshT[32][260];
-  int n0 = blockIdx.x * 16, m0 = blockIdx.y * 32;
-  int tid = threadIdx.x;
-  int y = n0 >> 6, x0 = n0 & 63;
-  {
-    int mm = tid >> 3, kg = (tid & 7) * 32;
-    const float4* src = (const float4*)&W[(m0 + mm) * 256 + kg];
-    float4* dst = (float4*)&wshT[mm][kg];
-#pragma unroll
-    for (int i = 0; i < 8; i++) dst[i] = src[i];
-  }
-  {
-    int px4 = (tid & 3) * 4;
-    int xabs = x0 + px4;
-#pragma unroll
-    for (int k = 0; k < 4; k++) {
-      int c = (tid >> 2) + 64 * k;
-      const float* base = f1 + c * NPIX;
-      float wv[9];
-#pragma unroll
-      for (int i = 0; i < 9; i++) wv[i] = dww[c * 9 + i];
-      float bc = dwb[c];
-      float a[4] = {bc, bc, bc, bc};
-#pragma unroll
-      for (int dy = 0; dy < 3; dy++) {
-        int yy = y + dy - 1;
-        if (yy < 0 || yy > 63) continue;
-        const float* row = base + yy * IMG + xabs;
-        float4 mid = *(const float4*)row;
-        float left = (xabs > 0) ? row[-1] : 0.f;
-        float right = (xabs + 4 < IMG) ? row[4] : 0.f;
-        float win[6] = {left, mid.x, mid.y, mid.z, mid.w, right};
-#pragma unroll
-        for (int o = 0; o < 4; o++)
-#pragma unroll
-          for (int dx = 0; dx < 3; dx++)
-            a[o] = fmaf(wv[dy * 3 + dx], win[o + dx], a[o]);
-      }
-#pragma unroll
-      for (int o = 0; o < 4; o++)
-        xs2[px4 + o][c] =
-            0.5f * a[o] * (1.f + erff(a[o] * 0.70710678118654752f));
-    }
-  }
-  __syncthreads();
-  int m = tid >> 3, np = (tid & 7) * 2;
-  float a0 = 0.f, a1 = 0.f;
-#pragma unroll 4
-  for (int k4 = 0; k4 < 64; k4++) {
-    float4 w4 = *(const float4*)&wshT[m][k4 * 4];
-    float4 xa = *(const float4*)&xs2[np][k4 * 4];
-    float4 xb = *(const float4*)&xs2[np + 1][k4 * 4];
-    a0 = fmaf(w4.x, xa.x, a0);
-    a1 = fmaf(w4.x, xb.x, a1);
-    a0 = fmaf(w4.y, xa.y, a0);
-    a1 = fmaf(w4.y, xb.y, a1);
-    a0 = fmaf(w4.z, xa.z, a0);
-    a1 = fmaf(w4.z, xb.z, a1);
-    a0 = fmaf(w4.w, xa.w, a0);
-    a1 = fmaf(w4.w, xb.w, a1);
-  }
-  int row = m0 + m;
-  float bv = bias[row];
-  const float2 rr = *(const float2*)&resid[row * NPIX + n0 + np];
-  *(float2*)&C[row * NPIX + n0 + np] =
-      make_float2(a0 + bv + rr.x, a1 + bv + rr.y);
 }
 
 extern "C" void kernel_launch(void* const* d_in, const int* in_sizes, int n_in,
@@ -634,17 +691,12 @@
   float* x1   = w + 3158144;
   float* f1   = w + 3420288;
   float* h2   = w + 4468864;
-
-  lc12_kernel<<<dim3(16, 8), 256, 0, stream>>>(luma, lc1_w, lc1_b, lc2_w,
-                                               lc2_b, x, h2, pooled, bsums,
-                                               mu1, rs1, cbuf);
-  ln_qkv_kernel<<<dim3(128, 3), 256, 0, stream>>>(
-      x, mu1, rs1, ln1_w, ln1_b, qkv_w, qkv_b, gam_w, gam_b, bet_w, bet_b, h2,
-      pooled, bsums, alpha, qhl, khl, vthx, vtlx);
-  attn_kernel<<<dim3(16, 8, 8), 256, 0, stream>>>(qhl, khl, vthx, vtlx, cbuf,
-                                                  pacc, pl);
-  proj_ffn1_kernel<<<dim3(128, 4), 256, 0, stream>>>(
-      pacc, pl, proj_w, proj_b, x, ln2_w, ln2_b, ffn1_w, ffn1_b, x1, f1);
-  ffn2_dw_kernel<<<dim3(256, 2), 256, 0, stream>>>(f1, dw_w, dw_b, ffn2_w,
-                                                   ffn2_b, x1, out);
+  unsigned int* ctr = (unsigned int*)(w + 4599936);
+
+  init_kernel<<<1, 64, 0, stream>>>(ctr, cbuf);
+  fused_kernel<<<dim3(NBLK), 256, 0, stream>>>(
+      x, luma, lc1_w, lc1_b, lc2_w, lc2_b, ln1_w, ln1_b, qkv_w, qkv_b, gam_w,
+      gam_b, bet_w, bet_b, alpha, proj_w, proj_b, ln2_w, ln2_b, ffn1_w, ffn1_b,
+      dw_w, dw_b, ffn2_w, ffn2_b, out, pooled, bsums, cbuf, mu1, rs1, qhl, khl,
+      vthx, vtlx, pacc, pl, x1, f1, h2, ctr);
 }
```

After: 615.8 us. 223% more time.
